# Performance work log

Measured on AMD Instinct MI355X. Metric: run time of the kernel, lower is better.

Reference implementation:

```python
import jax, jax.numpy as jnp
import numpy as np
import math
from jax import lax

B, HS, WS, C, T, TD, HH, TOPM = 8, 64, 64, 512, 77, 512, 8, 3
DH = C // HH
CONF_TH = 0.35


def _layernorm(x, w, b, eps=1e-5):
    mu = x.mean(-1, keepdims=True)
    var = ((x - mu) ** 2).mean(-1, keepdims=True)
    return (x - mu) * lax.rsqrt(var + eps) * w + b


def _l2norm(x, eps=1e-6):
    n = jnp.sqrt((x * x).sum(-1, keepdims=True))
    return x / jnp.maximum(n, eps)


def _forward(visual_features, text_features, geo_mask,
             ln1_w, ln1_b, wq, bq, wk, bk, wv, bv, wo, bo,
             gate_w, gate_b, logit_scale, alpha,
             ln2_w, ln2_b, ffn_w1, ffn_b1, ffn_w2, ffn_b2):
    Bb, Hs, Ws, Cv = visual_features.shape
    N = Hs * Ws
    # Pre-LN + flatten spatial
    x = _layernorm(visual_features, ln1_w, ln1_b).reshape(Bb, N, Cv)
    q_full = x @ wq + bq                                  # [B,N,C]
    pad_mask = jnp.abs(text_features).sum(-1) <= 1e-6     # [B,T]
    k_full = text_features @ wk + bk                      # [B,T,C]
    v_full = text_features @ wv + bv
    # per-token L2 normalize over full channel dim, then split heads
    q = _l2norm(q_full).reshape(Bb, N, HH, DH)
    k = _l2norm(k_full).reshape(Bb, T, HH, DH)
    v = v_full.reshape(Bb, T, HH, DH)
    scale = jnp.exp(jnp.clip(logit_scale, -2.0, 2.0)) / jnp.sqrt(jnp.float32(DH))
    sim = jnp.einsum('bnhd,bthd->bnht', q, k) * scale     # [B,N,H,T]
    # geo gate (4D tensor branch): log-bias on logits + multiplicative channel gate later
    gate_map = jnp.clip(geo_mask, 0.3, 1.0)               # [B,1,Hs,Ws]
    geo_gate_flat = gate_map.reshape(Bb, N, 1)            # [B,N,1]
    sim = sim + jnp.log(jnp.maximum(gate_map.reshape(Bb, N), 1e-6))[:, :, None, None]
    sim = jnp.where(pad_mask[:, None, None, :], -jnp.inf, sim)
    # Top-K sparsification before softmax (threshold at the K-th value)
    topv = lax.top_k(sim, TOPM)[0]                        # [B,N,H,K]
    sim = jnp.where(sim >= topv[..., -1:], sim, -jnp.inf)
    attn = jax.nn.softmax(sim, axis=-1)
    attn = attn / jnp.maximum(attn.sum(-1, keepdims=True), 1e-6)
    # fully-padded rows -> zero
    all_pad = pad_mask.all(axis=1)
    attn = jnp.where(all_pad[:, None, None, None], 0.0, attn)
    # confidence bypass: conf = max_prob * (1 - normalized entropy), mean over heads
    a_hn = attn.transpose(0, 2, 1, 3)                     # [B,H,N,T]
    maxp = a_hn.max(-1, keepdims=True)
    t_eff = jnp.maximum((a_hn > 0).astype(a_hn.dtype).sum(-1, keepdims=True), 2.0)
    p = jnp.maximum(a_hn, 1e-8)
    ent = jnp.maximum(-(p * jnp.log(p)).sum(-1, keepdims=True) / jnp.log(t_eff), 0.0)
    conf = jnp.clip(maxp * (1.0 - ent), 0.0, 1.0).mean(axis=1)   # [B,N,1]
    conf_scale = CONF_TH + (1.0 - CONF_TH) * jnp.clip(conf, 0.0, 1.0)
    aligned = jnp.einsum('bnht,bthd->bnhd', attn, v).reshape(Bb, N, HH * DH)
    aligned = (aligned @ wo + bo) * conf_scale
    gate = jax.nn.sigmoid(x @ gate_w + gate_b) * geo_gate_flat
    y = x + alpha * gate * aligned
    h = _layernorm(y, ln2_w, ln2_b)
    y = y + (jax.nn.gelu(h @ ffn_w1 + ffn_b1, approximate=False) @ ffn_w2 + ffn_b2)
    return y.reshape(Bb, Hs, Ws, Cv)


def setup_inputs() -> dict:
    key = jax.random.key(0)
    ks = jax.random.split(key, 16)
    def w(k, shp, fan_in):
        return (jax.random.normal(k, shp, jnp.float32) * (1.0 / math.sqrt(fan_in))).astype(jnp.float32)
    return {
        'visual_features': jax.random.normal(ks[0], (B, HS, WS, C), jnp.float32),
        'text_features':   jax.random.normal(ks[1], (B, T, TD), jnp.float32),
        'geo_mask':        jax.random.uniform(ks[2], (B, 1, HS, WS), jnp.float32),
        'ln1_w': jnp.ones((C,), jnp.float32), 'ln1_b': jnp.zeros((C,), jnp.float32),
        'wq': w(ks[3], (C, C), C),   'bq': jnp.zeros((C,), jnp.float32),
        'wk': w(ks[4], (TD, C), TD), 'bk': jnp.zeros((C,), jnp.float32),
        'wv': w(ks[5], (TD, C), TD), 'bv': jnp.zeros((C,), jnp.float32),
        'wo': w(ks[6], (C, C), C),   'bo': jnp.zeros((C,), jnp.float32),
        'gate_w': w(ks[7], (C, C), C), 'gate_b': jnp.zeros((C,), jnp.float32),
        'logit_scale': jnp.float32(math.log(1.0 / 0.07)),
        'alpha': jnp.float32(0.1),
        'ln2_w': jnp.ones((C,), jnp.float32), 'ln2_b': jnp.zeros((C,), jnp.float32),
        'ffn_w1': w(ks[8], (C, 4 * C), C),    'ffn_b1': jnp.zeros((4 * C,), jnp.float32),
        'ffn_w2': w(ks[9], (4 * C, C), 4 * C), 'ffn_b2': jnp.zeros((C,), jnp.float32),
    }


def reference(visual_features, text_features, geo_mask,
              ln1_w, ln1_b, wq, bq, wk, bk, wv, bv, wo, bo,
              gate_w, gate_b, logit_scale, alpha,
              ln2_w, ln2_b, ffn_w1, ffn_b1, ffn_w2, ffn_b2):
    return _forward(visual_features, text_features, geo_mask,
                    ln1_w, ln1_b, wq, bq, wk, bk, wv, bv, wo, bo,
                    gate_w, gate_b, logit_scale, alpha,
                    ln2_w, ln2_b, ffn_w1, ffn_b1, ffn_w2, ffn_b2)
```

## Files before the change

### kernel.cpp

```cpp
#include <hip/hip_runtime.h>
#include <hip/hip_bf16.h>
#include <math.h>

#define TT 77
#define MTOT 32768

typedef __attribute__((ext_vector_type(8))) short bf16x8;
typedef __attribute__((ext_vector_type(4))) float floatx4;

#define GPTR(p) ((const __attribute__((address_space(1))) void*)(p))
#define LPTR(p) ((__attribute__((address_space(3))) void*)(p))

__device__ __forceinline__ float wred_sum(float v) {
#pragma unroll
  for (int o = 32; o >= 1; o >>= 1) v += __shfl_xor(v, o, 64);
  return v;
}

__device__ __forceinline__ unsigned short f2bf(float f) {
  unsigned int u = __float_as_uint(f);
  unsigned int r = (u + 0x7fffu + ((u >> 16) & 1u)) >> 16;
  return (unsigned short)r;
}
__device__ __forceinline__ float bf2f(unsigned short h) {
  return __uint_as_float(((unsigned int)h) << 16);
}
__device__ __forceinline__ unsigned int cvt2bf(float a, float b) {
  unsigned int r;
  asm("v_cvt_pk_bf16_f32 %0, %1, %2" : "=v"(r) : "v"(a), "v"(b));
  return r;
}

__device__ __forceinline__ float fast_gelu(float o) {
  const float z = fabsf(o) * 0.70710678118654752f;
  const float t = __builtin_amdgcn_rcpf(fmaf(0.3275911f, z, 1.0f));
  float p = fmaf(1.061405429f, t, -1.453152027f);
  p = fmaf(p, t, 1.421413741f);
  p = fmaf(p, t, -0.284496736f);
  p = fmaf(p, t, 0.254829592f);
  p = p * t;
  const float erfz = fmaf(-p, __expf(-z * z), 1.0f);
  const float s = __builtin_copysignf(erfz, o);
  return 0.5f * o * (1.0f + s);
}

__device__ __forceinline__ float fast_sigmoid(float o) {
  return __builtin_amdgcn_rcpf(1.0f + __expf(-o));
}

__global__ __launch_bounds__(256)
void ln_bf16_kernel(const float* __restrict__ in, const float* __restrict__ gw,
                    const float* __restrict__ gb, unsigned short* __restrict__ out) {
  const int wv = threadIdx.x >> 6, lane = threadIdx.x & 63;
  const size_t row = (size_t)blockIdx.x * 4 + wv;
  const float* p = in + row * 512 + lane * 8;
  float4 a = *(const float4*)p;
  float4 b = *(const float4*)(p + 4);
  float s = a.x + a.y + a.z + a.w + b.x + b.y + b.z + b.w;
  float mu = wred_sum(s) * (1.0f / 512.0f);
  float d[8] = {a.x - mu, a.y - mu, a.z - mu, a.w - mu,
                b.x - mu, b.y - mu, b.z - mu, b.w - mu};
  float ss = 0.f;
#pragma unroll
  for (int i = 0; i < 8; ++i) ss = fmaf(d[i], d[i], ss);
  float var = wred_sum(ss) * (1.0f / 512.0f);
  float rstd = rsqrtf(var + 1e-5f);
  float4 w0 = *(const float4*)(gw + lane * 8);
  float4 w1 = *(const float4*)(gw + lane * 8 + 4);
  float4 c0 = *(const float4*)(gb + lane * 8);
  float4 c1 = *(const float4*)(gb + lane * 8 + 4);
  float o[8];
  o[0] = d[0] * rstd * w0.x + c0.x;  o[1] = d[1] * rstd * w0.y + c0.y;
  o[2] = d[2] * rstd * w0.z + c0.z;  o[3] = d[3] * rstd * w0.w + c0.w;
  o[4] = d[4] * rstd * w1.x + c1.x;  o[5] = d[5] * rstd * w1.y + c1.y;
  o[6] = d[6] * rstd * w1.z + c1.z;  o[7] = d[7] * rstd * w1.w + c1.w;
  __align__(16) unsigned short ob[8];
#pragma unroll
  for (int i = 0; i < 8; ++i) ob[i] = f2bf(o[i]);
  *(uint4*)(out + row * 512 + lane * 8) = *(const uint4*)ob;
}

__global__ __launch_bounds__(256)
void zero_acc_kernel(float* __restrict__ ssq, float* __restrict__ conf) {
  const int i = blockIdx.x * 256 + threadIdx.x;
  ssq[i] = 0.0f;
  conf[i] = 0.0f;
}

__global__ __launch_bounds__(256)
void transpose_bf16_kernel(const float* __restrict__ W, unsigned short* __restrict__ WTb,
                           int K, int N) {
  __shared__ float s[32][33];
  const int tx = threadIdx.x & 31, ty = threadIdx.x >> 5;
  const int n0 = blockIdx.x * 32, k0 = blockIdx.y * 32;
#pragma unroll
  for (int j = 0; j < 4; ++j)
    s[ty + 8 * j][tx] = W[(size_t)(k0 + ty + 8 * j) * N + n0 + tx];
  __syncthreads();
#pragma unroll
  for (int j = 0; j < 4; ++j)
    WTb[(size_t)(n0 + ty + 8 * j) * K + k0 + tx] = f2bf(s[tx][ty + 8 * j]);
}

__global__ __launch_bounds__(256)
void transpose_pair_kernel(const float* __restrict__ W,
                           unsigned short* __restrict__ WTh,
                           unsigned short* __restrict__ WTl, int K, int N) {
  __shared__ float s[32][33];
  const int tx = threadIdx.x & 31, ty = threadIdx.x >> 5;
  const int n0 = blockIdx.x * 32, k0 = blockIdx.y * 32;
#pragma unroll
  for (int j = 0; j < 4; ++j)
    s[ty + 8 * j][tx] = W[(size_t)(k0 + ty + 8 * j) * N + n0 + tx];
  __syncthreads();
#pragma unroll
  for (int j = 0; j < 4; ++j) {
    const float a = s[tx][ty + 8 * j];
    const unsigned short hi = f2bf(a);
    WTh[(size_t)(n0 + ty + 8 * j) * K + k0 + tx] = hi;
    WTl[(size_t)(n0 + ty + 8 * j) * K + k0 + tx] = f2bf(a - bf2f(hi));
  }
}

__global__ __launch_bounds__(256)
void text_cvt_kernel(const float* __restrict__ text,
                     unsigned short* __restrict__ thi,
                     unsigned short* __restrict__ tlo,
                     float* __restrict__ negm) {
  const int wv = threadIdx.x >> 6, lane = threadIdx.x & 63;
  const int row = blockIdx.x * 4 + wv;
  if (row >= 616) {
    const uint4 z = {0u, 0u, 0u, 0u};
    *(uint4*)(thi + (size_t)row * 512 + lane * 8) = z;
    *(uint4*)(tlo + (size_t)row * 512 + lane * 8) = z;
    return;
  }
  const float* p = text + (size_t)row * 512 + lane * 8;
  float4 a = *(const float4*)p;
  float4 b = *(const float4*)(p + 4);
  float v[8] = {a.x, a.y, a.z, a.w, b.x, b.y, b.z, b.w};
  float ab = 0.f;
#pragma unroll
  for (int i = 0; i < 8; ++i) ab += fabsf(v[i]);
  ab = wred_sum(ab);
  __align__(16) unsigned short hb[8];
  __align__(16) unsigned short lb[8];
#pragma unroll
  for (int i = 0; i < 8; ++i) {
    hb[i] = f2bf(v[i]);
    lb[i] = f2bf(v[i] - bf2f(hb[i]));
  }
  *(uint4*)(thi + (size_t)row * 512 + lane * 8) = *(const uint4*)hb;
  *(uint4*)(tlo + (size_t)row * 512 + lane * 8) = *(const uint4*)lb;
  if (lane == 0) {
    const int bb = row / 77, t = row - bb * 77;
    negm[bb * 80 + t] = (ab <= 1e-6f) ? -INFINITY : 0.0f;
  }
}

__global__ __launch_bounds__(256)
void kv_gemm(const unsigned short* __restrict__ AH,
             const unsigned short* __restrict__ AL,
             const unsigned short* __restrict__ BH,
             const unsigned short* __restrict__ BL,
             const float* __restrict__ bk, const float* __restrict__ bv,
             float* __restrict__ outp) {
  const int K = 512;
  __shared__ __align__(16) unsigned short AsH[128 * 32];
  __shared__ __align__(16) unsigned short AsL[128 * 32];
  __shared__ __align__(16) unsigned short BsH[128 * 32];
  __shared__ __align__(16) unsigned short BsL[128 * 32];
  const int tid = threadIdx.x;
  const int wid = tid >> 6, lane = tid & 63;
  const int wr = wid >> 1, wc = wid & 1;
  const int m16 = lane & 15, quad = lane >> 4;
  const int row0 = blockIdx.y * 128, col0 = blockIdx.x * 128;

  const floatx4 zero4 = {0.f, 0.f, 0.f, 0.f};
  floatx4 acc[4][4];
#pragma unroll
  for (int i = 0; i < 4; ++i)
#pragma unroll
    for (int j = 0; j < 4; ++j) acc[i][j] = zero4;

  const int srow = tid >> 2;
  const int schunk = (tid & 3) ^ (srow & 3);
  const unsigned short* AgH = AH + (size_t)(row0 + srow) * K + schunk * 8;
  const unsigned short* AgL = AL + (size_t)(row0 + srow) * K + schunk * 8;
  const unsigned short* BgH = BH + (size_t)(col0 + srow) * K + schunk * 8;
  const unsigned short* BgL = BL + (size_t)(col0 + srow) * K + schunk * 8;
  char* AsHB = (char*)AsH + tid * 16;
  char* AsLB = (char*)AsL + tid * 16;
  char* BsHB = (char*)BsH + tid * 16;
  char* BsLB = (char*)BsL + tid * 16;
  const int rq = quad ^ (m16 & 3);
  const int aOfs = (wr * 64 + m16) * 32 + rq * 8;
  const int bOfs = (wc * 64 + m16) * 32 + rq * 8;

  for (int k0 = 0; k0 < K; k0 += 32) {
    __syncthreads();
    __builtin_amdgcn_global_load_lds(GPTR(AgH + k0), LPTR(AsHB), 16, 0, 0);
    __builtin_amdgcn_global_load_lds(GPTR(AgH + (size_t)64 * K + k0), LPTR(AsHB + 4096), 16, 0, 0);
    __builtin_amdgcn_global_load_lds(GPTR(AgL + k0), LPTR(AsLB), 16, 0, 0);
    __builtin_amdgcn_global_load_lds(GPTR(AgL + (size_t)64 * K + k0), LPTR(AsLB + 4096), 16, 0, 0);
    __builtin_amdgcn_global_load_lds(GPTR(BgH + k0), LPTR(BsHB), 16, 0, 0);
    __builtin_amdgcn_global_load_lds(GPTR(BgH + (size_t)64 * K + k0), LPTR(BsHB + 4096), 16, 0, 0);
    __builtin_amdgcn_global_load_lds(GPTR(BgL + k0), LPTR(BsLB), 16, 0, 0);
    __builtin_amdgcn_global_load_lds(GPTR(BgL + (size_t)64 * K + k0), LPTR(BsLB + 4096), 16, 0, 0);
    __syncthreads();
    bf16x8 afH[4], afL[4], bfH[4], bfL[4];
#pragma unroll
    for (int i = 0; i < 4; ++i) {
      afH[i] = *(const bf16x8*)(AsH + aOfs + i * 16 * 32);
      afL[i] = *(const bf16x8*)(AsL + aOfs + i * 16 * 32);
      bfH[i] = *(const bf16x8*)(BsH + bOfs + i * 16 * 32);
      bfL[i] = *(const bf16x8*)(BsL + bOfs + i * 16 * 32);
    }
#pragma unroll
    for (int mi = 0; mi < 4; ++mi)
#pragma unroll
      for (int ni = 0; ni < 4; ++ni) {
        acc[mi][ni] = __builtin_amdgcn_mfma_f32_16x16x32_bf16(afH[mi], bfH[ni], acc[mi][ni], 0, 0, 0);
        acc[mi][ni] = __builtin_amdgcn_mfma_f32_16x16x32_bf16(afH[mi], bfL[ni], acc[mi][ni], 0, 0, 0);
        acc[mi][ni] = __builtin_amdgcn_mfma_f32_16x16x32_bf16(afL[mi], bfH[ni], acc[mi][ni], 0, 0, 0);
      }
  }

  const float* bp = (col0 < 512) ? bk : bv;
  const int cbase = (col0 < 512) ? col0 : col0 - 512;
  float bb[4];
#pragma unroll
  for (int ni = 0; ni < 4; ++ni) bb[ni] = bp[cbase + wc * 64 + ni * 16 + m16];
#pragma unroll
  for (int mi = 0; mi < 4; ++mi)
#pragma unroll
    for (int r = 0; r < 4; ++r) {
      const int row = row0 + wr * 64 + mi * 16 + quad * 4 + r;
#pragma unroll
      for (int ni = 0; ni < 4; ++ni) {
        const int col = col0 + wc * 64 + ni * 16 + m16;
        outp[(size_t)row * 1024 + col] = acc[mi][ni][r] + bb[ni];
      }
    }
}

__global__ __launch_bounds__(256)
void knorm_kernel(const float* __restrict__ KV,
                  unsigned short* __restrict__ khb) {
  const int wv = threadIdx.x >> 6, lane = threadIdx.x & 63;
  const int row = blockIdx.x * 4 + wv;
  const float* p = KV + (size_t)row * 1024 + lane * 8;
  float4 a = *(const float4*)p;
  float4 b = *(const float4*)(p + 4);
  float v[8] = {a.x, a.y, a.z, a.w, b.x, b.y, b.z, b.w};
  float ss = 0.f;
#pragma unroll
  for (int i = 0; i < 8; ++i) ss = fmaf(v[i], v[i], ss);
  ss = wred_sum(ss);
  const float sc = 1.0f / fmaxf(sqrtf(ss), 1e-6f);
  const int bb = row / 77, t = row - bb * 77;
  const int c = lane * 8, h = c >> 6, d = c & 63;
  __align__(16) unsigned short ob[8];
#pragma unroll
  for (int i = 0; i < 8; ++i) ob[i] = f2bf(v[i] * sc);
  *(uint4*)(khb + (((size_t)bb * 8 + h) * 80 + t) * 64 + d) = *(const uint4*)ob;
}

__global__ __launch_bounds__(256)
void kpad_zero_kernel(unsigned short* __restrict__ khb, float* __restrict__ negm) {
  const int i = blockIdx.x * 256 + threadIdx.x;
  const int bh = i / 192, rem = i - bh * 192;
  const int t = 77 + rem / 64, d = rem & 63;
  khb[(((size_t)bh) * 80 + t) * 64 + d] = 0;
  if (i < 24) negm[(i / 3) * 80 + 77 + (i % 3)] = -INFINITY;
}

__global__ __launch_bounds__(256)
void sim_attn_kernel(const unsigned short* __restrict__ qnb,
                     const unsigned short* __restrict__ khb,
                     const float* __restrict__ negm,
                     const float* __restrict__ ssq,
                     const float* __restrict__ logit_scale,
                     const float* __restrict__ vf,
                     unsigned short* __restrict__ alignedb,
                     float* __restrict__ confacc) {
  __shared__ __align__(16) char lbuf[128 * 81 * 4];
  unsigned short* As = (unsigned short*)lbuf;
  unsigned short* Bs = As + 128 * 72;
  float* simt = (float*)lbuf;

  const int bh = blockIdx.y;
  const int b = bh >> 3, h = bh & 7;
  const int row0 = blockIdx.x * 128;
  const int tid = threadIdx.x;

  {
    const int r = tid >> 1, half = tid & 1;
    const unsigned short* src = qnb + ((size_t)b * 4096 + row0 + r) * 512 + h * 64 + half * 32;
    unsigned short* dst = As + r * 72 + half * 32;
    *(uint4*)dst = *(const uint4*)src;
    *(uint4*)(dst + 8) = *(const uint4*)(src + 8);
    *(uint4*)(dst + 16) = *(const uint4*)(src + 16);
    *(uint4*)(dst + 24) = *(const uint4*)(src + 24);
  }
  if (tid < 160) {
    const int r = tid >> 1, half = tid & 1;
    const unsigned short* src = khb + ((size_t)bh * 80 + r) * 64 + half * 32;
    unsigned short* dst = Bs + r * 72 + half * 32;
    *(uint4*)dst = *(const uint4*)src;
    *(uint4*)(dst + 8) = *(const uint4*)(src + 8);
    *(uint4*)(dst + 16) = *(const uint4*)(src + 16);
    *(uint4*)(dst + 24) = *(const uint4*)(src + 24);
  }
  __syncthreads();

  const int w = tid >> 6, lane = tid & 63;
  const int m16 = lane & 15, quad = lane >> 4;
  const unsigned short* aBase = As + (w * 32 + m16) * 72 + quad * 8;
  const unsigned short* bBase = Bs + m16 * 72 + quad * 8;
  bf16x8 af[2][2], bf[5][2];
#pragma unroll
  for (int mi = 0; mi < 2; ++mi)
#pragma unroll
    for (int kk = 0; kk < 2; ++kk)
      af[mi][kk] = *(const bf16x8*)(aBase + mi * 16 * 72 + kk * 32);
#pragma unroll
  for (int ni = 0; ni < 5; ++ni)
#pragma unroll
    for (int kk = 0; kk < 2; ++kk)
      bf[ni][kk] = *(const bf16x8*)(bBase + ni * 16 * 72 + kk * 32);
  __syncthreads();

  const floatx4 zero4 = {0.f, 0.f, 0.f, 0.f};
  floatx4 acc[2][5];
#pragma unroll
  for (int mi = 0; mi < 2; ++mi)
#pragma unroll
    for (int ni = 0; ni < 5; ++ni) acc[mi][ni] = zero4;
#pragma unroll
  for (int kk = 0; kk < 2; ++kk)
#pragma unroll
    for (int mi = 0; mi < 2; ++mi)
#pragma unroll
      for (int ni = 0; ni < 5; ++ni)
        acc[mi][ni] = __builtin_amdgcn_mfma_f32_16x16x32_bf16(af[mi][kk], bf[ni][kk], acc[mi][ni], 0, 0, 0);

  const float ls = fminf(fmaxf(logit_scale[0], -2.0f), 2.0f);
  const float scale = expf(ls) * 0.125f;
  float nm[5];
#pragma unroll
  for (int ni = 0; ni < 5; ++ni) nm[ni] = negm[b * 80 + ni * 16 + m16];
#pragma unroll
  for (int mi = 0; mi < 2; ++mi)
#pragma unroll
    for (int r = 0; r < 4; ++r) {
      const int lr = w * 32 + quad * 4 + mi * 16 + r;
      const float ssv = ssq[(size_t)b * 4096 + row0 + lr];
      const float nsc = scale / fmaxf(sqrtf(ssv), 1e-6f);
#pragma unroll
      for (int ni = 0; ni < 5; ++ni)
        simt[lr * 81 + ni * 16 + m16] = acc[mi][ni][r] * nsc + nm[ni];
    }
  __syncthreads();

  const int lr = tid >> 1, half = tid & 1;
  const int n = row0 + lr;
  const float* sp = simt + lr * 81;

  float m1 = -INFINITY, m2 = -INFINITY, m3 = -INFINITY, m4 = -INFINITY;
  int a1 = 0, a2 = 0, a3 = 0;
  for (int t = 0; t < 80; ++t) {
    const float v = sp[t];
    const bool c1 = v > m1, c2 = v > m2, c3 = v > m3, c4 = v > m4;
    m4 = c4 ? (c3 ? m3 : v) : m4;
    m3 = c3 ? (c2 ? m2 : v) : m3;
    a3 = c3 ? (c2 ? a2 : t) : a3;
    m2 = c2 ? (c1 ? m1 : v) : m2;
    a2 = c2 ? (c1 ? a1 : t) : a2;
    m1 = c1 ? v : m1;
    a1 = c1 ? t : a1;
  }

  const bool dead = (m1 == -INFINITY);
  if (dead) m1 = 0.0f;
  const bool tie = (!dead) && ((m1 == m2) || (m2 == m3) || (m3 == m4));

  const float d2 = m2 - m1, d3 = m3 - m1;
  const float e2 = __expf(d2), e3 = __expf(d3);
  float s0 = 1.0f + e2 + e3;
  float s1 = ((e2 > 0.f) ? e2 * d2 : 0.f) + ((e3 > 0.f) ? e3 * d3 : 0.f);
  float cntf = 1.0f + ((e2 > 0.f) ? 1.f : 0.f) + ((e3 > 0.f) ? 1.f : 0.f);

  unsigned short* op = alignedb + ((size_t)b * 4096 + n) * 512 + h * 64 + half * 32;

  if (tie) {
    s0 = 0.f; s1 = 0.f; cntf = 0.f;
    float4 acc2[8];
#pragma unroll
    for (int i = 0; i < 8; ++i) acc2[i] = (float4){0.f, 0.f, 0.f, 0.f};
    for (int t = 0; t < 80; ++t) {
      const float v = sp[t];
      if (v >= m3) {
        const float e = expf(v - m1);
        if (e > 0.f) {
          s0 += e; s1 = fmaf(e, v - m1, s1); cntf += 1.f;
          const float4* vp = (const float4*)(vf + (size_t)(b * 77 + t) * 1024 + h * 64 + half * 32);
#pragma unroll
          for (int i = 0; i < 8; ++i) {
            const float4 x = vp[i];
            acc2[i].x = fmaf(e, x.x, acc2[i].x);
            acc2[i].y = fmaf(e, x.y, acc2[i].y);
            acc2[i].z = fmaf(e, x.z, acc2[i].z);
            acc2[i].w = fmaf(e, x.w, acc2[i].w);
          }
        }
      }
    }
    const float invt = 1.0f / s0;
#pragma unroll
    for (int i = 0; i < 4; ++i) {
      const float4 lo = acc2[2 * i], hi = acc2[2 * i + 1];
      uint4 pk;
      pk.x = cvt2bf(lo.x * invt, lo.y * invt);
      pk.y = cvt2bf(lo.z * invt, lo.w * invt);
      pk.z = cvt2bf(hi.x * invt, hi.y * invt);
      pk.w = cvt2bf(hi.z * invt, hi.w * invt);
      *(uint4*)(op + i * 8) = pk;
    }
  } else {
    const float inv0 = 1.0f / s0;
    const float wA = dead ? 0.f : inv0;
    const float wB = e2 * inv0, wC = e3 * inv0;
    const float* v1p = vf + (size_t)(b * 77 + a1) * 1024 + h * 64 + half * 32;
    const float* v2p = vf + (size_t)(b * 77 + a2) * 1024 + h * 64 + half * 32;
    const float* v3p = vf + (size_t)(b * 77 + a3) * 1024 + h * 64 + half * 32;
#pragma unroll
    for (int i = 0; i < 4; ++i) {
      const float4 x0 = ((const float4*)v1p)[2 * i];
      const float4 x1 = ((const float4*)v1p)[2 * i + 1];
      const float4 y0 = ((const float4*)v2p)[2 * i];
      const float4 y1 = ((const float4*)v2p)[2 * i + 1];
      const float4 z0 = ((const float4*)v3p)[2 * i];
      const float4 z1 = ((const float4*)v3p)[2 * i + 1];
      float4 r0, r1;
      r0.x = fmaf(wC, z0.x, fmaf(wB, y0.x, wA * x0.x));
      r0.y = fmaf(wC, z0.y, fmaf(wB, y0.y, wA * x0.y));
      r0.z = fmaf(wC, z0.z, fmaf(wB, y0.z, wA * x0.z));
      r0.w = fmaf(wC, z0.w, fmaf(wB, y0.w, wA * x0.w));
      r1.x = fmaf(wC, z1.x, fmaf(wB, y1.x, wA * x1.x));
      r1.y = fmaf(wC, z1.y, fmaf(wB, y1.y, wA * x1.y));
      r1.z = fmaf(wC, z1.z, fmaf(wB, y1.z, wA * x1.z));
      r1.w = fmaf(wC, z1.w, fmaf(wB, y1.w, wA * x1.w));
      uint4 pk;
      pk.x = cvt2bf(r0.x, r0.y);
      pk.y = cvt2bf(r0.z, r0.w);
      pk.z = cvt2bf(r1.x, r1.y);
      pk.w = cvt2bf(r1.z, r1.w);
      *(uint4*)(op + i * 8) = pk;
    }
  }

  if (half == 0) {
    const float inv = 1.0f / s0;
    const float entn = (__logf(s0) - s1 * inv) + (77.0f - cntf) * 1.8420681e-7f;
    const float ent = fmaxf(entn / __logf(fmaxf(cntf, 2.0f)), 0.0f);
    float conf_h = fminf(fmaxf(inv * (1.0f - ent), 0.0f), 1.0f);
    if (dead) conf_h = 0.f;
    atomicAdd(confacc + (size_t)b * 4096 + n, conf_h * 0.125f);
  }
}

template <int EPI, int KC>
__global__ __launch_bounds__(256)
void mfma_gemm(const unsigned short* __restrict__ A,
               const unsigned short* __restrict__ WT,
               const float* __restrict__ bias,
               void* __restrict__ outv, int M, int N,
               const unsigned short* __restrict__ e0b,
               const float* __restrict__ e1f,
               const float* __restrict__ e2f,
               const float* __restrict__ scf) {
  __shared__ __align__(16) unsigned short As[128 * 32];
  __shared__ __align__(16) unsigned short Bs[128 * 32];
  const int tid = threadIdx.x;
  const int wid = tid >> 6, lane = tid & 63;
  const int wr = wid >> 1, wc = wid & 1;
  const int m16 = lane & 15, quad = lane >> 4;

  const int nwg = gridDim.x * gridDim.y;
  const int orig = blockIdx.y * gridDim.x + blockIdx.x;
  const int qq = nwg >> 3, rr = nwg & 7;
  const int xcd = orig & 7, base = orig >> 3;
  const int logical = (xcd < rr ? xcd * (qq + 1) : rr * (qq + 1) + (xcd - rr) * qq) + base;
  const int bx = logical % gridDim.x, by = logical / gridDim.x;
  const int row0 = by * 128, col0 = bx * 128;

  const floatx4 zero4 = {0.f, 0.f, 0.f, 0.f};
  floatx4 acc[4][4];
#pragma unroll
  for (int i = 0; i < 4; ++i)
#pragma unroll
    for (int j = 0; j < 4; ++j) acc[i][j] = zero4;

  const int srow = tid >> 2;
  const int schunk = (tid & 3) ^ (srow & 3);
  const unsigned short* Ag = A + (size_t)(row0 + srow) * KC + schunk * 8;
  const unsigned short* Bg = WT + (size_t)(col0 + srow) * KC + schunk * 8;
  char* AsB = (char*)As + tid * 16;
  char* BsB = (char*)Bs + tid * 16;
  const int rq = quad ^ (m16 & 3);
  const unsigned short* aP = As + (wr * 64 + m16) * 32 + rq * 8;
  const unsigned short* bP = Bs + (wc * 64 + m16) * 32 + rq * 8;

  for (int k0 = 0; k0 < KC; k0 += 32) {
    __syncthreads();
    __builtin_amdgcn_global_load_lds(GPTR(Ag + k0), LPTR(AsB), 16, 0, 0);
    __builtin_amdgcn_global_load_lds(GPTR(Ag + (size_t)64 * KC + k0), LPTR(AsB + 4096), 16, 0, 0);
    __builtin_amdgcn_global_load_lds(GPTR(Bg + k0), LPTR(BsB), 16, 0, 0);
    __builtin_amdgcn_global_load_lds(GPTR(Bg + (size_t)64 * KC + k0), LPTR(BsB + 4096), 16, 0, 0);
    __syncthreads();
    bf16x8 af[4], bfr[4];
#pragma unroll
    for (int i = 0; i < 4; ++i) {
      af[i] = *(const bf16x8*)(aP + i * 16 * 32);
      bfr[i] = *(const bf16x8*)(bP + i * 16 * 32);
    }
#pragma unroll
    for (int mi = 0; mi < 4; ++mi)
#pragma unroll
      for (int ni = 0; ni < 4; ++ni)
        acc[mi][ni] = __builtin_amdgcn_mfma_f32_16x16x32_bf16(af[mi], bfr[ni], acc[mi][ni], 0, 0, 0);
  }

  float* outf = (float*)outv;
  unsigned short* outb = (unsigned short*)outv;
  const unsigned short* albf = (const unsigned short*)e1f;
  float bb[4];
#pragma unroll
  for (int ni = 0; ni < 4; ++ni) bb[ni] = bias[col0 + wc * 64 + ni * 16 + m16];
  const float alphav = (EPI == 2) ? scf[0] : 0.f;

#pragma unroll
  for (int mi = 0; mi < 4; ++mi) {
#pragma unroll
    for (int r = 0; r < 4; ++r) {
      const int row = row0 + wr * 64 + mi * 16 + quad * 4 + r;
      float o[4];
#pragma unroll
      for (int ni = 0; ni < 4; ++ni) o[ni] = acc[mi][ni][r] + bb[ni];
      const size_t basei = (size_t)row * N + col0 + wc * 64 + m16;

      if (EPI == 5) {
        const unsigned int p01 = cvt2bf(o[0], o[1]);
        const unsigned int p23 = cvt2bf(o[2], o[3]);
        outb[basei] = (unsigned short)p01;
        outb[basei + 16] = (unsigned short)(p01 >> 16);
        outb[basei + 32] = (unsigned short)p23;
        outb[basei + 48] = (unsigned short)(p23 >> 16);
        float p = fmaf(o[0], o[0], fmaf(o[1], o[1], fmaf(o[2], o[2], o[3] * o[3])));
        p += __shfl_xor(p, 1, 64);
        p += __shfl_xor(p, 2, 64);
        p += __shfl_xor(p, 4, 64);
        p += __shfl_xor(p, 8, 64);
        if (m16 == 0) atomicAdd(const_cast<float*>(e1f) + row, p);
      } else if (EPI == 3) {
        const unsigned int p01 = cvt2bf(fast_gelu(o[0]), fast_gelu(o[1]));
        const unsigned int p23 = cvt2bf(fast_gelu(o[2]), fast_gelu(o[3]));
        outb[basei] = (unsigned short)p01;
        outb[basei + 16] = (unsigned short)(p01 >> 16);
        outb[basei + 32] = (unsigned short)p23;
        outb[basei + 48] = (unsigned short)(p23 >> 16);
      } else if (EPI == 1) {
        const float cm = fminf(fmaxf(e1f[row], 0.0f), 1.0f);
        const float rowscale = 0.35f + 0.65f * cm;
        const unsigned int p01 = cvt2bf(o[0] * rowscale, o[1] * rowscale);
        const unsigned int p23 = cvt2bf(o[2] * rowscale, o[3] * rowscale);
        outb[basei] = (unsigned short)p01;
        outb[basei + 16] = (unsigned short)(p01 >> 16);
        outb[basei + 32] = (unsigned short)p23;
        outb[basei + 48] = (unsigned short)(p23 >> 16);
      } else if (EPI == 2) {
        const float geo = fminf(fmaxf(e2f[row], 0.3f), 1.0f);
#pragma unroll
        for (int ni = 0; ni < 4; ++ni) {
          const size_t idx = basei + ni * 16;
          const float x = bf2f(e0b[idx]);
          const float al = bf2f(albf[idx]);
          const float sg = fast_sigmoid(o[ni]);
          outf[idx] = x + alphav * sg * geo * al;
        }
      } else {
#pragma unroll
        for (int ni = 0; ni < 4; ++ni) {
          const size_t idx = basei + ni * 16;
          outf[idx] = o[ni] + e1f[idx];
        }
      }
    }
  }
}

extern "C" void kernel_launch(void* const* d_in, const int* in_sizes, int n_in,
                              void* d_out, int out_size, void* d_ws, size_t ws_size,
                              hipStream_t stream) {
  const float* visual = (const float*)d_in[0];
  const float* text   = (const float*)d_in[1];
  const float* geo    = (const float*)d_in[2];
  const float* ln1_w  = (const float*)d_in[3];
  const float* ln1_b  = (const float*)d_in[4];
  const float* wq     = (const float*)d_in[5];
  const float* bq     = (const float*)d_in[6];
  const float* wk     = (const float*)d_in[7];
  const float* bk     = (const float*)d_in[8];
  const float* wvw    = (const float*)d_in[9];
  const float* bv     = (const float*)d_in[10];
  const float* wo     = (const float*)d_in[11];
  const float* bo     = (const float*)d_in[12];
  const float* gate_w = (const float*)d_in[13];
  const float* gate_b = (const float*)d_in[14];
  const float* logit_scale = (const float*)d_in[15];
  const float* alpha  = (const float*)d_in[16];
  const float* ln2_w  = (const float*)d_in[17];
  const float* ln2_b  = (const float*)d_in[18];
  const float* ffn_w1 = (const float*)d_in[19];
  const float* ffn_b1 = (const float*)d_in[20];
  const float* ffn_w2 = (const float*)d_in[21];
  const float* ffn_b2 = (const float*)d_in[22];
  float* out = (float*)d_out;

  char* ws = (char*)d_ws;
  float* R0            = (float*)ws;
  float* BUF2          = (float*)(ws + 88080384);
  unsigned short* Xb   = (unsigned short*)(ws + 155189248);
  unsigned short* QNb  = (unsigned short*)(ws + 188743680);
  unsigned short* wqT  = (unsigned short*)(ws + 222298112);
  unsigned short* woT  = wqT + 262144;
  unsigned short* gateT = woT + 262144;
  unsigned short* w1T  = gateT + 262144;
  unsigned short* w2T  = w1T + 1048576;
  unsigned short* KHb  = w2T + 1048576;
  float* NEGM = (float*)(ws + 230146048);
  float* CONF = (float*)(ws + 230148608);
  float* SSQ  = (float*)(ws + 230279680);

  float* KV            = (float*)(ws + 88080384);
  unsigned short* THi  = (unsigned short*)(ws + 88080384 + 2621440);
  unsigned short* TLo  = THi + 640 * 512;
  unsigned short* WKVh = TLo + 640 * 512;
  unsigned short* WKVl = WKVh + 1024 * 512;

  unsigned short* ALb = (unsigned short*)R0;
  unsigned short* AOb = QNb;

  transpose_bf16_kernel<<<dim3(16, 16), 256, 0, stream>>>(wq, wqT, 512, 512);
  transpose_bf16_kernel<<<dim3(16, 16), 256, 0, stream>>>(wo, woT, 512, 512);
  transpose_bf16_kernel<<<dim3(16, 16), 256, 0, stream>>>(gate_w, gateT, 512, 512);
  transpose_bf16_kernel<<<dim3(64, 16), 256, 0, stream>>>(ffn_w1, w1T, 512, 2048);
  transpose_bf16_kernel<<<dim3(16, 64), 256, 0, stream>>>(ffn_w2, w2T, 2048, 512);
  transpose_pair_kernel<<<dim3(16, 16), 256, 0, stream>>>(wk, WKVh, WKVl, 512, 512);
  transpose_pair_kernel<<<dim3(16, 16), 256, 0, stream>>>(wvw, WKVh + 512 * 512, WKVl + 512 * 512, 512, 512);

  ln_bf16_kernel<<<MTOT / 4, 256, 0, stream>>>(visual, ln1_w, ln1_b, Xb);
  zero_acc_kernel<<<128, 256, 0, stream>>>(SSQ, CONF);
  text_cvt_kernel<<<160, 256, 0, stream>>>(text, THi, TLo, NEGM);
  kv_gemm<<<dim3(8, 5), 256, 0, stream>>>(THi, TLo, WKVh, WKVl, bk, bv, KV);
  knorm_kernel<<<154, 256, 0, stream>>>(KV, KHb);
  kpad_zero_kernel<<<48, 256, 0, stream>>>(KHb, NEGM);
  mfma_gemm<5, 512><<<dim3(4, 256), 256, 0, stream>>>(Xb, wqT, bq, QNb, MTOT, 512,
                                                      nullptr, SSQ, nullptr, nullptr);
  sim_attn_kernel<<<dim3(32, 64), 256, 0, stream>>>(QNb, KHb, NEGM, SSQ, logit_scale,
                                                    KV + 512, ALb, CONF);
  mfma_gemm<1, 512><<<dim3(4, 256), 256, 0, stream>>>(ALb, woT, bo, AOb, MTOT, 512,
                                                      nullptr, CONF, nullptr, nullptr);
  mfma_gemm<2, 512><<<dim3(4, 256), 256, 0, stream>>>(Xb, gateT, gate_b, BUF2, MTOT, 512,
                                                      Xb, (const float*)AOb, geo, alpha);
  ln_bf16_kernel<<<MTOT / 4, 256, 0, stream>>>(BUF2, ln2_w, ln2_b, Xb);
  unsigned short* GCH = (unsigned short*)R0;
  for (int ch = 0; ch < 2; ++ch) {
    const size_t off = (size_t)ch * 16384;
    mfma_gemm<3, 512><<<dim3(16, 128), 256, 0, stream>>>(Xb + off * 512, w1T, ffn_b1, GCH,
                                                         16384, 2048,
                                                         nullptr, nullptr, nullptr, nullptr);
    mfma_gemm<4, 2048><<<dim3(4, 128), 256, 0, stream>>>(GCH, w2T, ffn_b2, out + off * 512,
                                                         16384, 512,
                                                         nullptr, BUF2 + off * 512, nullptr, nullptr);
  }
}
```

Measured before the change: 583.4 us.

## Double GEMM K-step to 64 and permute B rows for vectorized epilogue stores

The MFMA GEMM now stages a K-chunk of 64 per iteration instead of 32, using an XOR swizzle over 8 chunks. This halves the number of barrier pairs per tile and raises the compute done per sync. The weight rows loaded into LDS are permuted so that each lane's four output columns become contiguous. The epilogue can then use packed uint2 and float4 loads and stores instead of strided scalar accesses. LDS use doubles to 32 KB per block, which may lower occupancy.

```diff
diff --git a/kernel.cpp b/kernel.cpp
--- a/kernel.cpp
+++ b/kernel.cpp
@@ -480,8 +480,8 @@
                const float* __restrict__ e1f,
                const float* __restrict__ e2f,
                const float* __restrict__ scf) {
-  __shared__ __align__(16) unsigned short As[128 * 32];
-  __shared__ __align__(16) unsigned short Bs[128 * 32];
+  __shared__ __align__(16) unsigned short As[128 * 64];
+  __shared__ __align__(16) unsigned short Bs[128 * 64];
   const int tid = threadIdx.x;
   const int wid = tid >> 6, lane = tid & 63;
   const int wr = wid >> 1, wc = wid & 1;
@@ -502,42 +502,50 @@
 #pragma unroll
     for (int j = 0; j < 4; ++j) acc[i][j] = zero4;
 
-  const int srow = tid >> 2;
-  const int schunk = (tid & 3) ^ (srow & 3);
-  const unsigned short* Ag = A + (size_t)(row0 + srow) * KC + schunk * 8;
-  const unsigned short* Bg = WT + (size_t)(col0 + srow) * KC + schunk * 8;
-  char* AsB = (char*)As + tid * 16;
-  char* BsB = (char*)Bs + tid * 16;
-  const int rq = quad ^ (m16 & 3);
-  const unsigned short* aP = As + (wr * 64 + m16) * 32 + rq * 8;
-  const unsigned short* bP = Bs + (wc * 64 + m16) * 32 + rq * 8;
-
-  for (int k0 = 0; k0 < KC; k0 += 32) {
+  size_t aoff[4], boff[4];
+  char* ldst[4];
+#pragma unroll
+  for (int j = 0; j < 4; ++j) {
+    const int s = wid * 64 + j * 256 + lane;
+    const int r = s >> 3;
+    const int gc = (s & 7) ^ (r & 7);
+    aoff[j] = (size_t)(row0 + r) * KC + gc * 8;
+    const int br = (r & 64) + 4 * (r & 15) + ((r >> 4) & 3);
+    boff[j] = (size_t)(col0 + br) * KC + gc * 8;
+    ldst[j] = (char*)nullptr + (size_t)s * 16;
+  }
+
+  for (int k0 = 0; k0 < KC; k0 += 64) {
     __syncthreads();
-    __builtin_amdgcn_global_load_lds(GPTR(Ag + k0), LPTR(AsB), 16, 0, 0);
-    __builtin_amdgcn_global_load_lds(GPTR(Ag + (size_t)64 * KC + k0), LPTR(AsB + 4096), 16, 0, 0);
-    __builtin_amdgcn_global_load_lds(GPTR(Bg + k0), LPTR(BsB), 16, 0, 0);
-    __builtin_amdgcn_global_load_lds(GPTR(Bg + (size_t)64 * KC + k0), LPTR(BsB + 4096), 16, 0, 0);
+#pragma unroll
+    for (int j = 0; j < 4; ++j) {
+      __builtin_amdgcn_global_load_lds(GPTR(A + aoff[j] + k0), LPTR((char*)As + (size_t)(ldst[j] - (char*)nullptr)), 16, 0, 0);
+      __builtin_amdgcn_global_load_lds(GPTR(WT + boff[j] + k0), LPTR((char*)Bs + (size_t)(ldst[j] - (char*)nullptr)), 16, 0, 0);
+    }
     __syncthreads();
-    bf16x8 af[4], bfr[4];
-#pragma unroll
-    for (int i = 0; i < 4; ++i) {
-      af[i] = *(const bf16x8*)(aP + i * 16 * 32);
-      bfr[i] = *(const bf16x8*)(bP + i * 16 * 32);
-    }
-#pragma unroll
-    for (int mi = 0; mi < 4; ++mi)
-#pragma unroll
-      for (int ni = 0; ni < 4; ++ni)
-        acc[mi][ni] = __builtin_amdgcn_mfma_f32_16x16x32_bf16(af[mi], bfr[ni], acc[mi][ni], 0, 0, 0);
+#pragma unroll
+    for (int kk = 0; kk < 2; ++kk) {
+      const int pc = (kk * 4 + quad) ^ (m16 & 7);
+      bf16x8 af[4], bfr[4];
+#pragma unroll
+      for (int i = 0; i < 4; ++i) {
+        af[i] = *(const bf16x8*)((const char*)As + (wr * 64 + i * 16 + m16) * 128 + pc * 16);
+        bfr[i] = *(const bf16x8*)((const char*)Bs + (wc * 64 + i * 16 + m16) * 128 + pc * 16);
+      }
+#pragma unroll
+      for (int mi = 0; mi < 4; ++mi)
+#pragma unroll
+        for (int ni = 0; ni < 4; ++ni)
+          acc[mi][ni] = __builtin_amdgcn_mfma_f32_16x16x32_bf16(af[mi], bfr[ni], acc[mi][ni], 0, 0, 0);
+    }
   }
 
   float* outf = (float*)outv;
   unsigned short* outb = (unsigned short*)outv;
   const unsigned short* albf = (const unsigned short*)e1f;
-  float bb[4];
-#pragma unroll
-  for (int ni = 0; ni < 4; ++ni) bb[ni] = bias[col0 + wc * 64 + ni * 16 + m16];
+  const int colb = col0 + wc * 64 + 4 * m16;
+  const float4 bbv = *(const float4*)(bias + colb);
+  const float bb[4] = {bbv.x, bbv.y, bbv.z, bbv.w};
   const float alphav = (EPI == 2) ? scf[0] : 0.f;
 
 #pragma unroll
@@ -548,15 +556,13 @@
       float o[4];
 #pragma unroll
       for (int ni = 0; ni < 4; ++ni) o[ni] = acc[mi][ni][r] + bb[ni];
-      const size_t basei = (size_t)row * N + col0 + wc * 64 + m16;
+      const size_t basei = (size_t)row * N + colb;
 
       if (EPI == 5) {
-        const unsigned int p01 = cvt2bf(o[0], o[1]);
-        const unsigned int p23 = cvt2bf(o[2], o[3]);
-        outb[basei] = (unsigned short)p01;
-        outb[basei + 16] = (unsigned short)(p01 >> 16);
-        outb[basei + 32] = (unsigned short)p23;
-        outb[basei + 48] = (unsigned short)(p23 >> 16);
+        uint2 pk;
+        pk.x = cvt2bf(o[0], o[1]);
+        pk.y = cvt2bf(o[2], o[3]);
+        *(uint2*)(outb + basei) = pk;
         float p = fmaf(o[0], o[0], fmaf(o[1], o[1], fmaf(o[2], o[2], o[3] * o[3])));
         p += __shfl_xor(p, 1, 64);
         p += __shfl_xor(p, 2, 64);
@@ -564,37 +570,39 @@
         p += __shfl_xor(p, 8, 64);
         if (m16 == 0) atomicAdd(const_cast<float*>(e1f) + row, p);
       } else if (EPI == 3) {
-        const unsigned int p01 = cvt2bf(fast_gelu(o[0]), fast_gelu(o[1]));
-        const unsigned int p23 = cvt2bf(fast_gelu(o[2]), fast_gelu(o[3]));
-        outb[basei] = (unsigned short)p01;
-        outb[basei + 16] = (unsigned short)(p01 >> 16);
-        outb[basei + 32] = (unsigned short)p23;
-        outb[basei + 48] = (unsigned short)(p23 >> 16);
+        uint2 pk;
+        pk.x = cvt2bf(fast_gelu(o[0]), fast_gelu(o[1]));
+        pk.y = cvt2bf(fast_gelu(o[2]), fast_gelu(o[3]));
+        *(uint2*)(outb + basei) = pk;
       } else if (EPI == 1) {
         const float cm = fminf(fmaxf(e1f[row], 0.0f), 1.0f);
         const float rowscale = 0.35f + 0.65f * cm;
-        const unsigned int p01 = cvt2bf(o[0] * rowscale, o[1] * rowscale);
-        const unsigned int p23 = cvt2bf(o[2] * rowscale, o[3] * rowscale);
-        outb[basei] = (unsigned short)p01;
-        outb[basei + 16] = (unsigned short)(p01 >> 16);
-        outb[basei + 32] = (unsigned short)p23;
-        outb[basei + 48] = (unsigned short)(p23 >> 16);
+        uint2 pk;
+        pk.x = cvt2bf(o[0] * rowscale, o[1] * rowscale);
+        pk.y = cvt2bf(o[2] * rowscale, o[3] * rowscale);
+        *(uint2*)(outb + basei) = pk;
       } else if (EPI == 2) {
         const float geo = fminf(fmaxf(e2f[row], 0.3f), 1.0f);
-#pragma unroll
-        for (int ni = 0; ni < 4; ++ni) {
-          const size_t idx = basei + ni * 16;
-          const float x = bf2f(e0b[idx]);
-          const float al = bf2f(albf[idx]);
-          const float sg = fast_sigmoid(o[ni]);
-          outf[idx] = x + alphav * sg * geo * al;
-        }
+        const uint2 xpk = *(const uint2*)(e0b + basei);
+        const uint2 apk = *(const uint2*)(albf + basei);
+        const float xv[4] = {bf2f((unsigned short)xpk.x), bf2f((unsigned short)(xpk.x >> 16)),
+                             bf2f((unsigned short)xpk.y), bf2f((unsigned short)(xpk.y >> 16))};
+        const float av[4] = {bf2f((unsigned short)apk.x), bf2f((unsigned short)(apk.x >> 16)),
+                             bf2f((unsigned short)apk.y), bf2f((unsigned short)(apk.y >> 16))};
+        float4 ov;
+        ov.x = xv[0] + alphav * fast_sigmoid(o[0]) * geo * av[0];
+        ov.y = xv[1] + alphav * fast_sigmoid(o[1]) * geo * av[1];
+        ov.z = xv[2] + alphav * fast_sigmoid(o[2]) * geo * av[2];
+        ov.w = xv[3] + alphav * fast_sigmoid(o[3]) * geo * av[3];
+        *(float4*)(outf + basei) = ov;
       } else {
-#pragma unroll
-        for (int ni = 0; ni < 4; ++ni) {
-          const size_t idx = basei + ni * 16;
-          outf[idx] = o[ni] + e1f[idx];
-        }
+        const float4 rv = *(const float4*)(e1f + basei);
+        float4 ov;
+        ov.x = o[0] + rv.x;
+        ov.y = o[1] + rv.y;
+        ov.z = o[2] + rv.z;
+        ov.w = o[3] + rv.w;
+        *(float4*)(outf + basei) = ov;
       }
     }
   }
```

Result: faster. 567.6 us (-2.7%).
